# Optimization experiments

Measured on AMD Instinct MI355X. Metric: run time of the kernel, lower is better.

Reference implementation:

```python
import jax, jax.numpy as jnp
import numpy as np

L_CHUNK = 5   # frames per camera chunk (hardcoded L=5 in similarity())
N_CAMS = 6    # len(cam_list)
TOP_K = 8     # hardcoded K=8 in similarity()
HEADS = 8


def setup_inputs() -> dict:
    key = jax.random.key(0)
    ks = jax.random.split(key, 5)
    B, M, N, C = 1, L_CHUNK * N_CAMS, 261, 2048  # M = S*P = 30 multiview token groups
    scale = 0.02
    tokens = jax.random.normal(ks[0], (B, M, N, C), dtype=jnp.float32)
    Wq = jax.random.normal(ks[1], (C, C), dtype=jnp.float32) * scale
    Wk = jax.random.normal(ks[2], (C, C), dtype=jnp.float32) * scale
    Wv = jax.random.normal(ks[3], (C, C), dtype=jnp.float32) * scale
    Wo = jax.random.normal(ks[4], (C, C), dtype=jnp.float32) * scale
    return {"tokens": tokens, "Wq": Wq, "Wk": Wk, "Wv": Wv, "Wo": Wo}


def _similarity(pose_tokens):
    # pose_tokens: [B, M, C] -> block-diag-biased softmax sim + topk neighbors
    sim = jnp.einsum('bmc,bnc->bmn', pose_tokens, pose_tokens)
    block = jnp.kron(jnp.eye(N_CAMS, dtype=sim.dtype),
                     jnp.ones((L_CHUNK, L_CHUNK), dtype=sim.dtype))  # [M, M]
    sim = sim + 10000.0 * block
    probs = jax.nn.softmax(sim, axis=-1)
    vals, idx = jax.lax.top_k(probs, TOP_K)  # [B, M, K]
    return vals, idx


def reference(tokens, Wq, Wk, Wv, Wo):
    B, M, N, C = tokens.shape
    H = HEADS
    d = C // H
    # similarity + topk over camera/pose tokens (token index 0 of each group)
    vals, idx = _similarity(tokens[:, :, 0, :])
    # gather K neighbor token groups per (batch, group): [B, M, K, N, C]
    nbr = jax.vmap(lambda t, i: t[i])(tokens, idx)
    nbr = nbr.reshape(B, M, TOP_K * N, C)
    q = (tokens @ Wq).reshape(B, M, N, H, d)
    k = (nbr @ Wk).reshape(B, M, TOP_K * N, H, d)
    v = (nbr @ Wv).reshape(B, M, TOP_K * N, H, d)
    scores = jnp.einsum('bmqhd,bmkhd->bmhqk', q, k) / jnp.sqrt(jnp.asarray(d, q.dtype))
    # weight each neighbor's tokens by its topk similarity value (log-bias)
    bias = jnp.repeat(jnp.log(vals + 1e-6), N, axis=-1)  # [B, M, K*N]
    scores = scores + bias[:, :, None, None, :]
    attn = jax.nn.softmax(scores, axis=-1)
    out = jnp.einsum('bmhqk,bmkhd->bmqhd', attn, v).reshape(B, M, N, C)
    return tokens + out @ Wo
```

## Files before the change

kernel.cpp:

```cpp
#include <hip/hip_runtime.h>
#include <stdint.h>

#define MTOK 7830
#define MPAD 7936
#define CD   2048
#define VTC  7920
#define AS1 __attribute__((address_space(1)))
#define AS3 __attribute__((address_space(3)))

typedef unsigned short u16;
typedef __bf16 bf16x8 __attribute__((ext_vector_type(8)));
typedef float f32x4 __attribute__((ext_vector_type(4)));
typedef unsigned short u16x8 __attribute__((ext_vector_type(8)));

__device__ __forceinline__ u16 f2bf(float f) {
  unsigned x = __float_as_uint(f);
  return (u16)((x + 0x7fffu + ((x >> 16) & 1u)) >> 16);
}

__device__ __forceinline__ void gld16(const u16* g, u16* l) {
  __builtin_amdgcn_global_load_lds((AS1 const unsigned int*)(g), (AS3 unsigned int*)(l), 16, 0, 0);
}

__global__ void cvt_tokens(const float* __restrict__ T, u16* __restrict__ O) {
  int row = blockIdx.x;
  size_t base = (size_t)row * CD + threadIdx.x * 8;
  u16x8 o = {0,0,0,0,0,0,0,0};
  if (row < MTOK) {
    const float* s = T + base;
    #pragma unroll
    for (int j = 0; j < 8; ++j) o[j] = f2bf(s[j]);
  }
  *(u16x8*)&O[base] = o;
}

__global__ void cvt_w(const float* __restrict__ Wq, const float* __restrict__ Wk,
                      const float* __restrict__ Wv, const float* __restrict__ Wo,
                      u16* __restrict__ WqkvT, u16* __restrict__ WoT) {
  __shared__ float tile[32][33];
  int k0 = blockIdx.x * 32;
  int n0 = blockIdx.y * 32;
  const float* W; u16* Dst; int nl0, dr0;
  if (n0 < 2048)      { W = Wq; Dst = WqkvT; nl0 = n0;        dr0 = n0; }
  else if (n0 < 4096) { W = Wk; Dst = WqkvT; nl0 = n0 - 2048; dr0 = n0; }
  else if (n0 < 6144) { W = Wv; Dst = WqkvT; nl0 = n0 - 4096; dr0 = n0; }
  else                { W = Wo; Dst = WoT;   nl0 = n0 - 6144; dr0 = n0 - 6144; }
  int tx = threadIdx.x, ty = threadIdx.y;
  #pragma unroll
  for (int i = 0; i < 4; ++i)
    tile[ty + i*8][tx] = W[(size_t)(k0 + ty + i*8) * CD + nl0 + tx];
  __syncthreads();
  #pragma unroll
  for (int i = 0; i < 4; ++i) {
    int n = ty + i*8;
    Dst[(size_t)(dr0 + n) * CD + k0 + tx] = f2bf(tile[tx][n]);
  }
}

__global__ void posesim(const float* __restrict__ tok, float* __restrict__ sim) {
  int mm = blockIdx.y, nn = blockIdx.x;
  const float* a = tok + (size_t)mm * 261 * CD;
  const float* b = tok + (size_t)nn * 261 * CD;
  int tid = threadIdx.x;
  float p = 0.f;
  for (int j = tid; j < CD; j += 256) p += a[j] * b[j];
  __shared__ float red[256];
  red[tid] = p; __syncthreads();
  for (int s = 128; s > 0; s >>= 1) { if (tid < s) red[tid] += red[tid + s]; __syncthreads(); }
  if (tid == 0) sim[mm*30 + nn] = red[0] + (((mm/5) == (nn/5)) ? 10000.0f : 0.0f);
}

__global__ void topk_bias(const float* __restrict__ sim, float* __restrict__ bias,
                          int* __restrict__ idxo) {
  int m = threadIdx.x;
  if (m >= 30) return;
  float p[30];
  float mx = -1e30f;
  for (int j = 0; j < 30; ++j) { p[j] = sim[m*30 + j]; mx = fmaxf(mx, p[j]); }
  float z = 0.f;
  for (int j = 0; j < 30; ++j) { p[j] = __expf(p[j] - mx); z += p[j]; }
  float inv = 1.0f / z;
  for (int j = 0; j < 30; ++j) p[j] *= inv;
  for (int k = 0; k < 8; ++k) {
    int bj = 0; float bv = p[0];
    for (int j = 1; j < 30; ++j) if (p[j] > bv) { bv = p[j]; bj = j; }
    idxo[m*8 + k] = bj;
    bias[m*8 + k] = logf(bv + 1e-6f);
    p[bj] = -1.0f;
  }
}

template<int EPI>
__global__ __launch_bounds__(256) void gemm_bt(
    const u16* __restrict__ A, const u16* __restrict__ Bt,
    u16* __restrict__ Cq, u16* __restrict__ Cv,
    const float* __restrict__ resid, float* __restrict__ Dout, int K)
{
  __shared__ u16 Al[128 * 64];
  __shared__ u16 Bl[128 * 64];
  int tid = threadIdx.x, lane = tid & 63, wid = tid >> 6;
  int lo4 = lane & 15, hi2 = lane >> 4;
  int bn = blockIdx.x, bm = blockIdx.y;
  int wy = wid >> 1, wx = wid & 1;
  int r8 = lane >> 3, c8 = lane & 7;
  f32x4 acc[4][4] = {};
  int nK = K >> 6;
  for (int t = 0; t < nK; ++t) {
    int k0 = t << 6;
    __syncthreads();
    #pragma unroll
    for (int i = 0; i < 4; ++i) {
      int ch = wid * 4 + i;
      int row = ch * 8 + r8;
      int sw = 8 * (c8 ^ (row & 7));
      gld16(A + (size_t)(bm*128 + row) * K + k0 + sw, &Al[ch * 512]);
      gld16(Bt + (size_t)(bn*128 + row) * K + k0 + sw, &Bl[ch * 512]);
    }
    __syncthreads();
    #pragma unroll
    for (int kk = 0; kk < 2; ++kk) {
      bf16x8 av[4], bv[4];
      #pragma unroll
      for (int mi = 0; mi < 4; ++mi) {
        int ar = wy*64 + mi*16 + lo4;
        av[mi] = *(const bf16x8*)&Al[ar*64 + 8*((hi2 + 4*kk) ^ (ar & 7))];
      }
      #pragma unroll
      for (int ni = 0; ni < 4; ++ni) {
        int br = wx*64 + ni*16 + lo4;
        bv[ni] = *(const bf16x8*)&Bl[br*64 + 8*((hi2 + 4*kk) ^ (br & 7))];
      }
      #pragma unroll
      for (int mi = 0; mi < 4; ++mi)
        #pragma unroll
        for (int ni = 0; ni < 4; ++ni)
          acc[mi][ni] = __builtin_amdgcn_mfma_f32_16x16x32_bf16(av[mi], bv[ni], acc[mi][ni], 0, 0, 0);
    }
  }
  int gm0 = bm*128 + wy*64;
  int gn0 = bn*128 + wx*64;
  #pragma unroll
  for (int mi = 0; mi < 4; ++mi) {
    #pragma unroll
    for (int ni = 0; ni < 4; ++ni) {
      int gmb = gm0 + mi*16 + hi2*4;
      int gn  = gn0 + ni*16 + lo4;
      #pragma unroll
      for (int r = 0; r < 4; ++r) {
        float v = acc[mi][ni][r];
        int gm = gmb + r;
        if (EPI == 0) {
          if (gn < 4096) {
            Cq[(size_t)gm * 4096 + gn] = f2bf(v);
          } else if (gm < MTOK) {
            int g = gm / 261, tk = gm - g * 261;
            Cv[(size_t)(gn - 4096) * VTC + g * 264 + tk] = f2bf(v);
          }
        } else {
          if (gm < MTOK) {
            size_t off = (size_t)gm * CD + gn;
            Dout[off] = resid[off] + v;
          }
        }
      }
    }
  }
}

__global__ __launch_bounds__(1024) void attn_main(
    const u16* __restrict__ QK,
    const u16* __restrict__ VtG,
    const float* __restrict__ bias, const int* __restrict__ idx,
    u16* __restrict__ AO)
{
  int h = blockIdx.x, m = blockIdx.y;
  int tid = threadIdx.x, lane = tid & 63, wid = tid >> 6;
  int lo4 = lane & 15, hi2 = lane >> 4;

  __shared__ u16 Kl[2][32 * 256];
  __shared__ u16 Vl[2][256 * 32];
  __shared__ u16 Pl[16][16 * 50];
  __shared__ float bias_s[8];
  __shared__ int   idx_s[8];
  if (tid < 8) {
    bias_s[tid] = bias[m*8 + tid] * 1.4426950408889634f;
    idx_s[tid]  = idx[m*8 + tid];
  }

  int qrow = m*261 + wid*16 + lo4;
  bf16x8 qf[8];
  #pragma unroll
  for (int kk = 0; kk < 8; ++kk)
    qf[kk] = *(const bf16x8*)&QK[(size_t)qrow * 4096 + h*256 + kk*32 + hi2*8];

  int rt = 2*wid + (lane >> 5);
  size_t kof = (size_t)rt * 4096 + 2048 + h*256 + 8*((lane & 31) ^ (rt & 7));
  int vdr = 16*wid + (lane >> 2);
  size_t vof = (size_t)(h*256 + vdr) * VTC + 8*((lane & 3) ^ ((vdr >> 1) & 3));

  f32x4 O[16] = {};
  float srun[4] = {0.f, 0.f, 0.f, 0.f};
  const float SC = 0.09016844f;

  {
    int ig0 = idx[m*8];
    gld16(QK + (size_t)(ig0*261) * 4096 + kof, &Kl[0][wid*512]);
    gld16(VtG + (size_t)(ig0*264) + vof,       &Vl[0][wid*512]);
  }

  int vswz = 8 * (hi2 ^ ((lo4 >> 1) & 3));
  int kxb  = (lo4 >> 2) & 1;
  int kswz = 8 * (hi2 ^ (lo4 & 3));

  for (int it = 0; it < 72; ++it) {
    __syncthreads();
    if (it + 1 < 72) {
      int tn = it + 1;
      int gg = tn / 9;
      int tok0n = (tn - gg*9) * 32;
      int ign = idx_s[gg];
      gld16(QK + (size_t)(ign*261 + tok0n) * 4096 + kof, &Kl[tn & 1][wid*512]);
      gld16(VtG + (size_t)(ign*264 + tok0n) + vof,       &Vl[tn & 1][wid*512]);
    }
    {
      int gg = it / 9;
      int tok0 = (it - gg*9) * 32;
      float bgl = bias_s[gg];
      const u16* Kb = Kl[it & 1];
      const u16* Vb = Vl[it & 1];

      f32x4 s0v = {0,0,0,0}, s1v = {0,0,0,0};
      __builtin_amdgcn_s_setprio(1);
      #pragma unroll
      for (int kk = 0; kk < 8; ++kk) {
        int off = lo4*256 + 32*(kk ^ kxb) + kswz;
        bf16x8 kb0 = *(const bf16x8*)&Kb[off];
        bf16x8 kb1 = *(const bf16x8*)&Kb[off + 16*256];
        s0v = __builtin_amdgcn_mfma_f32_16x16x32_bf16(qf[kk], kb0, s0v, 0, 0, 0);
        s1v = __builtin_amdgcn_mfma_f32_16x16x32_bf16(qf[kk], kb1, s1v, 0, 0, 0);
      }
      __builtin_amdgcn_s_setprio(0);
      bool v0 = (tok0 + lo4) < 261, v1 = (tok0 + 16 + lo4) < 261;
      float p0[4], p1[4];
      #pragma unroll
      for (int r = 0; r < 4; ++r) {
        float e0 = __builtin_exp2f(fmaf(s0v[r], SC, bgl));
        float e1 = __builtin_exp2f(fmaf(s1v[r], SC, bgl));
        e0 = v0 ? e0 : 0.f;
        e1 = v1 ? e1 : 0.f;
        srun[r] += e0 + e1;
        p0[r] = e0; p1[r] = e1;
      }
      u16* Pw = Pl[wid];
      #pragma unroll
      for (int r = 0; r < 4; ++r) {
        Pw[(hi2*4 + r)*50 + lo4]      = f2bf(p0[r]);
        Pw[(hi2*4 + r)*50 + 16 + lo4] = f2bf(p1[r]);
      }
      bf16x8 pa = *(const bf16x8*)&Pw[lo4*50 + hi2*8];
      __builtin_amdgcn_s_setprio(1);
      #pragma unroll
      for (int o = 0; o < 16; ++o) {
        bf16x8 vv = *(const bf16x8*)&Vb[(o*16 + lo4)*32 + vswz];
        O[o] = __builtin_amdgcn_mfma_f32_16x16x32_bf16(pa, vv, O[o], 0, 0, 0);
      }
      __builtin_amdgcn_s_setprio(0);
    }
  }

  #pragma unroll
  for (int r = 0; r < 4; ++r) {
    float s = srun[r];
    s += __shfl_xor(s, 1);
    s += __shfl_xor(s, 2);
    s += __shfl_xor(s, 4);
    s += __shfl_xor(s, 8);
    srun[r] = 1.0f / s;
  }
  #pragma unroll
  for (int o = 0; o < 16; ++o) {
    #pragma unroll
    for (int r = 0; r < 4; ++r) {
      int qq = wid*16 + hi2*4 + r;
      AO[(size_t)(m*261 + qq) * CD + h*256 + o*16 + lo4] = f2bf(O[o][r] * srun[r]);
    }
  }
}

__global__ __launch_bounds__(256) void attn_tail(
    const u16* __restrict__ QK, const u16* __restrict__ VtG,
    const float* __restrict__ bias, const int* __restrict__ idx,
    u16* __restrict__ AO)
{
  int h = blockIdx.x, m = blockIdx.y;
  int tid = threadIdx.x, lane = tid & 63, wid = tid >> 6;
  int lo4 = lane & 15, hi2 = lane >> 4;

  __shared__ float Om[4][16][256];
  __shared__ float Sm[4][16];
  __shared__ u16 Pl[4][16 * 50];

  int q = 256 + lo4;
  bool qv = q < 261;
  int qrow = m*261 + (qv ? q : 0);
  bf16x8 qf[8];
  #pragma unroll
  for (int kk = 0; kk < 8; ++kk) {
    u16x8 u = {0,0,0,0,0,0,0,0};
    if (qv) u = *(const u16x8*)&QK[(size_t)qrow * 4096 + h*256 + kk*32 + hi2*8];
    qf[kk] = __builtin_bit_cast(bf16x8, u);
  }

  f32x4 O[16] = {};
  float srun[4] = {0.f, 0.f, 0.f, 0.f};
  const float SC = 0.09016844f;

  for (int it = wid; it < 72; it += 4) {
    int gg = it / 9;
    int tok0 = (it - gg*9) * 32;
    int ig = idx[m*8 + gg];
    float bgl = bias[m*8 + gg] * 1.4426950408889634f;
    const u16* kbase = QK + (size_t)(ig*261 + tok0) * 4096 + 2048 + h*256;
    f32x4 s0v = {0,0,0,0}, s1v = {0,0,0,0};
    #pragma unroll
    for (int kk = 0; kk < 8; ++kk) {
      bf16x8 kb0 = *(const bf16x8*)&kbase[(size_t)lo4 * 4096 + kk*32 + hi2*8];
      bf16x8 kb1 = *(const bf16x8*)&kbase[(size_t)(16 + lo4) * 4096 + kk*32 + hi2*8];
      s0v = __builtin_amdgcn_mfma_f32_16x16x32_bf16(qf[kk], kb0, s0v, 0, 0, 0);
      s1v = __builtin_amdgcn_mfma_f32_16x16x32_bf16(qf[kk], kb1, s1v, 0, 0, 0);
    }
    bool v0 = (tok0 + lo4) < 261, v1 = (tok0 + 16 + lo4) < 261;
    float p0[4], p1[4];
    #pragma unroll
    for (int r = 0; r < 4; ++r) {
      float e0 = __builtin_exp2f(fmaf(s0v[r], SC, bgl));
      float e1 = __builtin_exp2f(fmaf(s1v[r], SC, bgl));
      e0 = v0 ? e0 : 0.f;
      e1 = v1 ? e1 : 0.f;
      srun[r] += e0 + e1;
      p0[r] = e0; p1[r] = e1;
    }
    u16* Pw = Pl[wid];
    #pragma unroll
    for (int r = 0; r < 4; ++r) {
      Pw[(hi2*4 + r)*50 + lo4]      = f2bf(p0[r]);
      Pw[(hi2*4 + r)*50 + 16 + lo4] = f2bf(p1[r]);
    }
    bf16x8 pa = *(const bf16x8*)&Pw[lo4*50 + hi2*8];
    const u16* vbase = VtG + (size_t)(h*256) * VTC + ig*264 + tok0;
    #pragma unroll
    for (int o = 0; o < 16; ++o) {
      bf16x8 vv = *(const bf16x8*)&vbase[(size_t)(o*16 + lo4) * VTC + hi2*8];
      O[o] = __builtin_amdgcn_mfma_f32_16x16x32_bf16(pa, vv, O[o], 0, 0, 0);
    }
  }

  #pragma unroll
  for (int r = 0; r < 4; ++r) {
    float s = srun[r];
    s += __shfl_xor(s, 1);
    s += __shfl_xor(s, 2);
    s += __shfl_xor(s, 4);
    s += __shfl_xor(s, 8);
    srun[r] = s;
  }
  #pragma unroll
  for (int o = 0; o < 16; ++o)
    #pragma unroll
    for (int r = 0; r < 4; ++r)
      Om[wid][hi2*4 + r][o*16 + lo4] = O[o][r];
  if (lo4 == 0) {
    #pragma unroll
    for (int r = 0; r < 4; ++r) Sm[wid][hi2*4 + r] = srun[r];
  }
  __syncthreads();
  if (wid == 0) {
    #pragma unroll
    for (int o = 0; o < 16; ++o) {
      #pragma unroll
      for (int r = 0; r < 4; ++r) {
        int row = hi2*4 + r;
        int qq = 256 + row;
        if (qq < 261) {
          int c = o*16 + lo4;
          float v = Om[0][row][c] + Om[1][row][c] + Om[2][row][c] + Om[3][row][c];
          float s = Sm[0][row] + Sm[1][row] + Sm[2][row] + Sm[3][row];
          AO[(size_t)(m*261 + qq) * CD + h*256 + c] = f2bf(v / s);
        }
      }
    }
  }
}

extern "C" void kernel_launch(void* const* d_in, const int* in_sizes, int n_in,
                              void* d_out, int out_size, void* d_ws, size_t ws_size,
                              hipStream_t stream) {
  const float* tokens = (const float*)d_in[0];
  const float* Wq = (const float*)d_in[1];
  const float* Wk = (const float*)d_in[2];
  const float* Wv = (const float*)d_in[3];
  const float* Wo = (const float*)d_in[4];
  float* out = (float*)d_out;
  char* ws = (char*)d_ws;

  constexpr size_t OFF_TOKBF = 0;
  constexpr size_t OFF_WQKVT = OFF_TOKBF + (size_t)MPAD * CD * 2;
  constexpr size_t OFF_WOT   = OFF_WQKVT + (size_t)6144 * CD * 2;
  constexpr size_t OFF_QK    = OFF_WOT   + (size_t)CD * CD * 2;
  constexpr size_t OFF_VTG   = OFF_QK    + (size_t)MPAD * 4096 * 2;
  constexpr size_t OFF_AO    = OFF_VTG   + (size_t)CD * VTC * 2 + 4096;
  constexpr size_t OFF_SIM   = OFF_AO    + (size_t)MPAD * CD * 2;
  constexpr size_t OFF_BIAS  = OFF_SIM   + 4096;
  constexpr size_t OFF_IDX   = OFF_BIAS  + 1024;

  u16* tokBf  = (u16*)(ws + OFF_TOKBF);
  u16* WqkvT  = (u16*)(ws + OFF_WQKVT);
  u16* WoT    = (u16*)(ws + OFF_WOT);
  u16* QKbuf  = (u16*)(ws + OFF_QK);
  u16* VtG    = (u16*)(ws + OFF_VTG);
  u16* attnO  = (u16*)(ws + OFF_AO);
  float* simw = (float*)(ws + OFF_SIM);
  float* bw   = (float*)(ws + OFF_BIAS);
  int*   iw   = (int*)(ws + OFF_IDX);

  cvt_tokens<<<MPAD, 256, 0, stream>>>(tokens, tokBf);
  cvt_w<<<dim3(64, 256), dim3(32, 8), 0, stream>>>(Wq, Wk, Wv, Wo, WqkvT, WoT);
  posesim<<<dim3(30, 30), 256, 0, stream>>>(tokens, simw);
  topk_bias<<<1, 32, 0, stream>>>(simw, bw, iw);
  gemm_bt<0><<<dim3(48, 62), 256, 0, stream>>>(tokBf, WqkvT, QKbuf, VtG, nullptr, nullptr, CD);
  attn_tail<<<dim3(8, 30), 256, 0, stream>>>(QKbuf, VtG, bw, iw, attnO);
  attn_main<<<dim3(8, 30), 1024, 0, stream>>>(QKbuf, VtG, bw, iw, attnO);
  gemm_bt<1><<<dim3(16, 62), 256, 0, stream>>>(attnO, WoT, nullptr, nullptr, tokens, out, CD);
}
```

Baseline: 752.4 us.

## Enlarge GEMM tiles to 256x256 with double-buffered LDS prefetch

The bf16 MFMA GEMM moves from 128x128 tiles with 4 waves to 256x256 tiles with 8 waves. Each wave now accumulates a 128x64 sub-tile. The LDS is double-buffered so the next K-slice's global_load_lds is issued while the current slice is multiplied, which drops one barrier per iteration. s_setprio is raised around the MFMA blocks. The intent is more data reuse per block and hiding load latency, at the cost of 128 KB of LDS per block, more registers and fewer blocks: 744 and 248 instead of 2976 and 992, which may underfill the 256 CUs on the output-projection GEMM.

```diff
diff --git a/kernel.cpp b/kernel.cpp
--- a/kernel.cpp
+++ b/kernel.cpp
@@ -91,56 +91,91 @@
 }
 
 template<int EPI>
-__global__ __launch_bounds__(256) void gemm_bt(
+__global__ __launch_bounds__(512) void gemm_bt(
     const u16* __restrict__ A, const u16* __restrict__ Bt,
     u16* __restrict__ Cq, u16* __restrict__ Cv,
     const float* __restrict__ resid, float* __restrict__ Dout, int K)
 {
-  __shared__ u16 Al[128 * 64];
-  __shared__ u16 Bl[128 * 64];
+  __shared__ u16 Al[2][256 * 64];
+  __shared__ u16 Bl[2][256 * 64];
   int tid = threadIdx.x, lane = tid & 63, wid = tid >> 6;
   int lo4 = lane & 15, hi2 = lane >> 4;
   int bn = blockIdx.x, bm = blockIdx.y;
-  int wy = wid >> 1, wx = wid & 1;
+  int wy = wid >> 2, wx = wid & 3;
   int r8 = lane >> 3, c8 = lane & 7;
-  f32x4 acc[4][4] = {};
+
+  f32x4 acc[8][4] = {};
+
+  size_t aofs[4], bofs[4];
+  #pragma unroll
+  for (int j = 0; j < 4; ++j) {
+    int row = wid*32 + j*8 + r8;
+    int sw = 8 * (c8 ^ (row & 7));
+    aofs[j] = (size_t)(bm*256 + row) * K + sw;
+    bofs[j] = (size_t)(bn*256 + row) * K + sw;
+  }
+  int ldst = wid * 2048;
+
   int nK = K >> 6;
+  #pragma unroll
+  for (int j = 0; j < 4; ++j) {
+    gld16(A  + aofs[j], &Al[0][ldst + j*512]);
+    gld16(Bt + bofs[j], &Bl[0][ldst + j*512]);
+  }
+
   for (int t = 0; t < nK; ++t) {
-    int k0 = t << 6;
     __syncthreads();
-    #pragma unroll
-    for (int i = 0; i < 4; ++i) {
-      int ch = wid * 4 + i;
-      int row = ch * 8 + r8;
-      int sw = 8 * (c8 ^ (row & 7));
-      gld16(A + (size_t)(bm*128 + row) * K + k0 + sw, &Al[ch * 512]);
-      gld16(Bt + (size_t)(bn*128 + row) * K + k0 + sw, &Bl[ch * 512]);
-    }
-    __syncthreads();
-    #pragma unroll
-    for (int kk = 0; kk < 2; ++kk) {
-      bf16x8 av[4], bv[4];
+    const u16* Ac = Al[t & 1];
+    const u16* Bc = Bl[t & 1];
+    u16* An = Al[(t + 1) & 1];
+    u16* Bn = Bl[(t + 1) & 1];
+    bool pf = (t + 1) < nK;
+    size_t kn = (size_t)(t + 1) << 6;
+
+    bf16x8 bvk[4];
+    #pragma unroll
+    for (int p = 0; p < 4; ++p) {
+      int kk = p >> 1, mg = p & 1;
+      if (p == 0 && pf) {
+        gld16(A  + kn + aofs[0], &An[ldst]);
+        gld16(A  + kn + aofs[1], &An[ldst + 512]);
+        gld16(Bt + kn + bofs[0], &Bn[ldst]);
+        gld16(Bt + kn + bofs[1], &Bn[ldst + 512]);
+      }
+      if (p == 1 && pf) {
+        gld16(A  + kn + aofs[2], &An[ldst + 1024]);
+        gld16(A  + kn + aofs[3], &An[ldst + 1536]);
+        gld16(Bt + kn + bofs[2], &Bn[ldst + 1024]);
+        gld16(Bt + kn + bofs[3], &Bn[ldst + 1536]);
+      }
+      if (mg == 0) {
+        #pragma unroll
+        for (int ni = 0; ni < 4; ++ni) {
+          int br = wx*64 + ni*16 + lo4;
+          bvk[ni] = *(const bf16x8*)&Bc[br*64 + 8*((kk*4 + hi2) ^ (br & 7))];
+        }
+      }
+      bf16x8 av[4];
       #pragma unroll
       for (int mi = 0; mi < 4; ++mi) {
-        int ar = wy*64 + mi*16 + lo4;
-        av[mi] = *(const bf16x8*)&Al[ar*64 + 8*((hi2 + 4*kk) ^ (ar & 7))];
-      }
-      #pragma unroll
-      for (int ni = 0; ni < 4; ++ni) {
-        int br = wx*64 + ni*16 + lo4;
-        bv[ni] = *(const bf16x8*)&Bl[br*64 + 8*((hi2 + 4*kk) ^ (br & 7))];
-      }
+        int ar = wy*128 + mg*64 + mi*16 + lo4;
+        av[mi] = *(const bf16x8*)&Ac[ar*64 + 8*((kk*4 + hi2) ^ (ar & 7))];
+      }
+      __builtin_amdgcn_s_setprio(1);
       #pragma unroll
       for (int mi = 0; mi < 4; ++mi)
         #pragma unroll
         for (int ni = 0; ni < 4; ++ni)
-          acc[mi][ni] = __builtin_amdgcn_mfma_f32_16x16x32_bf16(av[mi], bv[ni], acc[mi][ni], 0, 0, 0);
-    }
-  }
-  int gm0 = bm*128 + wy*64;
-  int gn0 = bn*128 + wx*64;
-  #pragma unroll
-  for (int mi = 0; mi < 4; ++mi) {
+          acc[mg*4 + mi][ni] =
+              __builtin_amdgcn_mfma_f32_16x16x32_bf16(av[mi], bvk[ni], acc[mg*4 + mi][ni], 0, 0, 0);
+      __builtin_amdgcn_s_setprio(0);
+    }
+  }
+
+  int gm0 = bm*256 + wy*128;
+  int gn0 = bn*256 + wx*64;
+  #pragma unroll
+  for (int mi = 0; mi < 8; ++mi) {
     #pragma unroll
     for (int ni = 0; ni < 4; ++ni) {
       int gmb = gm0 + mi*16 + hi2*4;
@@ -427,8 +462,8 @@
   cvt_w<<<dim3(64, 256), dim3(32, 8), 0, stream>>>(Wq, Wk, Wv, Wo, WqkvT, WoT);
   posesim<<<dim3(30, 30), 256, 0, stream>>>(tokens, simw);
   topk_bias<<<1, 32, 0, stream>>>(simw, bw, iw);
-  gemm_bt<0><<<dim3(48, 62), 256, 0, stream>>>(tokBf, WqkvT, QKbuf, VtG, nullptr, nullptr, CD);
+  gemm_bt<0><<<dim3(24, 31), 512, 0, stream>>>(tokBf, WqkvT, QKbuf, VtG, nullptr, nullptr, CD);
   attn_tail<<<dim3(8, 30), 256, 0, stream>>>(QKbuf, VtG, bw, iw, attnO);
   attn_main<<<dim3(8, 30), 1024, 0, stream>>>(QKbuf, VtG, bw, iw, attnO);
-  gemm_bt<1><<<dim3(16, 62), 256, 0, stream>>>(attnO, WoT, nullptr, nullptr, tokens, out, CD);
-}
+  gemm_bt<1><<<dim3(8, 31), 512, 0, stream>>>(attnO, WoT, nullptr, nullptr, tokens, out, CD);
+}
```

Result: no change. 742.0 us (-1.4%).
